# Performance work log

Measured on AMD Instinct MI355X. Metric: run time of the kernel, lower is better.

## Reference

```python
import jax, jax.numpy as jnp
import numpy as np

NUM_USERS = 50000
NUM_ITEMS = 100000
N_NODES = NUM_USERS + NUM_ITEMS
NNZ = 2400000
EMBED = 64
N_LAYERS = 3
BATCH = 4096
NEG_SLOPE = 0.2
EPS = 1e-12


def setup_inputs() -> dict:
    key = jax.random.key(0)
    ks = jax.random.split(key, 12)
    return {
        "edge_val": jax.random.uniform(ks[0], (NNZ,), jnp.float32) * 0.01,
        "embed_user": jax.random.normal(ks[1], (NUM_USERS, EMBED), jnp.float32) * 0.1,
        "embed_item": jax.random.normal(ks[2], (NUM_ITEMS, EMBED), jnp.float32) * 0.1,
        "W1_w": jax.random.normal(ks[3], (N_LAYERS, EMBED, EMBED), jnp.float32) * 0.2,
        "W1_b": jnp.zeros((N_LAYERS, EMBED), jnp.float32),
        "W2_w": jax.random.normal(ks[4], (N_LAYERS, EMBED, EMBED), jnp.float32) * 0.2,
        "W2_b": jnp.zeros((N_LAYERS, EMBED), jnp.float32),
        "edge_row": jax.random.randint(ks[5], (NNZ,), 0, N_NODES, jnp.int32),
        "edge_col": jax.random.randint(ks[6], (NNZ,), 0, N_NODES, jnp.int32),
        "batch_user": jax.random.randint(ks[7], (BATCH,), 0, NUM_USERS, jnp.int32),
        "batch_pos_item": jax.random.randint(ks[8], (BATCH,), 0, NUM_ITEMS, jnp.int32),
        "batch_neg_item": jax.random.randint(ks[9], (BATCH,), 0, NUM_ITEMS, jnp.int32),
    }


def _ngcf_embeddings(edge_val, embed_user, embed_item, W1_w, W1_b, W2_w, W2_b,
                     edge_row, edge_col):
    E = jnp.concatenate([embed_user, embed_item], axis=0)  # [N, d]
    embs = [E]
    for i in range(N_LAYERS):
        # SpMM: (L @ E)[r] = sum over edges e with row r of val[e] * E[col[e]]
        msgs = edge_val[:, None] * E[edge_col]  # [nnz, d]
        LE = jax.ops.segment_sum(msgs, edge_row, num_segments=N_NODES)
        # I is identity -> (L + I) @ E = LE + E
        ego = (LE + E) @ W1_w[i].T + W1_b[i]
        side = LE @ W2_w[i].T + W2_b[i]
        E = jax.nn.leaky_relu(ego + side, negative_slope=NEG_SLOPE)
        # message dropout p=0 is identity; L2-normalize per node (F.normalize)
        norm = jnp.linalg.norm(E, axis=1, keepdims=True)
        E = E / jnp.maximum(norm, EPS)
        embs.append(E)
    return jnp.concatenate(embs, axis=1)  # [N, (1+L)*d]


def reference(edge_val, embed_user, embed_item, W1_w, W1_b, W2_w, W2_b,
              edge_row, edge_col, batch_user, batch_pos_item, batch_neg_item):
    G = _ngcf_embeddings(edge_val, embed_user, embed_item, W1_w, W1_b, W2_w,
                         W2_b, edge_row, edge_col)
    user_g = G[:NUM_USERS]
    item_g = G[NUM_USERS:]
    return (user_g[batch_user], item_g[batch_pos_item], item_g[batch_neg_item])
```

## Files before the change

kernel.cpp:

```cpp
#include <hip/hip_runtime.h>
#include <hip/hip_fp16.h>

#define NUM_USERS 50000
#define NUM_ITEMS 100000
#define N_NODES   150000
#define EMBED     64
#define BATCH     4096
#define NNZ       2400000
#define NB        586
#define CBITS     10
#define NCOARSE   147
#define CAP       20480
#define TILE      4096
#define NTILES    9375

typedef _Float16 half8 __attribute__((ext_vector_type(8)));
typedef float    f32x4 __attribute__((ext_vector_type(4)));

__device__ __forceinline__ float bf2f(unsigned short u) {
    union { unsigned int u32; float f; } v; v.u32 = ((unsigned int)u) << 16; return v.f;
}
__device__ __forceinline__ float getf(const void* p, int i, int fbf) {
    if (fbf) return bf2f(((const unsigned short*)p)[i]);
    return ((const float*)p)[i];
}
__device__ __forceinline__ int geti(const void* p, int i, int i64) {
    if (i64) return (int)(((const long long*)p)[i]);
    return ((const int*)p)[i];
}
__device__ __forceinline__ int clampi(int v, int lo, int hi) {
    return v < lo ? lo : (v > hi ? hi : v);
}
__device__ __forceinline__ float h2f(unsigned short u) {
    return __half2float(__ushort_as_half(u));
}
__device__ __forceinline__ unsigned short f2h(float f) {
    return __half_as_ushort(__float2half(f));
}

__global__ void k_flags_r22(const unsigned short* __restrict__ ev,
                            const void* __restrict__ er, int* __restrict__ fl) {
    if (threadIdx.x == 0 && blockIdx.x == 0) {
        int good = 0;
        for (int i = 0; i < 64; ++i) {
            float f = bf2f(ev[i]);
            if (f >= 0.0f && f <= 0.011f) good++;
        }
        fl[0] = (good >= 60) ? 1 : 0;
        int ok = 0;
        for (int i = 0; i < 64; ++i) {
            long long v = ((const long long*)er)[i];
            if (v >= 0 && v < (long long)N_NODES) ok++;
        }
        fl[1] = (ok >= 60) ? 1 : 0;
    }
}

__global__ void k_probe_r22(int* __restrict__ fl) {
    __shared__ unsigned short A[16 * 32];
    __shared__ unsigned short B[32 * 16];
    const int lane = threadIdx.x;
    for (int i = lane; i < 512; i += 64) {
        int r = i >> 5, k = i & 31;
        A[i] = f2h(((r * 7 + k * 3) % 23) * 0.04f - 0.4f);
    }
    for (int i = lane; i < 512; i += 64) {
        int k = i >> 4, n = i & 15;
        B[i] = f2h(((k * 11 + n * 5) % 19) * 0.05f - 0.45f);
    }
    __syncthreads();
    union { unsigned short u[8]; half8 h; } ua, ub;
    const int rA = lane & 15;
    const int g  = lane >> 4;
    #pragma unroll
    for (int e = 0; e < 8; ++e) {
        ua.u[e] = A[rA * 32 + g * 8 + e];
        ub.u[e] = B[(g * 8 + e) * 16 + rA];
    }
    f32x4 acc = {0.f, 0.f, 0.f, 0.f};
    acc = __builtin_amdgcn_mfma_f32_16x16x32_f16(ua.h, ub.h, acc, 0, 0, 0);
    bool ok = true;
    #pragma unroll
    for (int reg = 0; reg < 4; ++reg) {
        int row = g * 4 + reg;
        int col = lane & 15;
        float ref = 0.0f;
        for (int k = 0; k < 32; ++k)
            ref += h2f(A[row * 32 + k]) * h2f(B[k * 16 + col]);
        if (fabsf(acc[reg] - ref) > 0.02f * fmaxf(1.0f, fabsf(ref))) ok = false;
    }
    unsigned long long m = __ballot(ok);
    if (lane == 0) fl[2] = (m == ~0ull) ? 1 : 0;
}

__global__ void k_init_r22(const void* __restrict__ eu, const void* __restrict__ ei,
                           const int* __restrict__ fl, unsigned short* __restrict__ Eh) {
    int fbf = fl[0];
    int i = blockIdx.x * 256 + threadIdx.x;
    if (i < N_NODES * EMBED) {
        int r = i >> 6;
        float v;
        if (r < NUM_USERS) v = getf(eu, i, fbf);
        else               v = getf(ei, i - NUM_USERS * EMBED, fbf);
        Eh[i] = f2h(v);
    }
}

__global__ __launch_bounds__(256) void k_partA_r22(const void* __restrict__ ev,
                                                   const void* __restrict__ er,
                                                   const void* __restrict__ ec,
                                                   const int* __restrict__ fl,
                                                   int* __restrict__ ccur,
                                                   int2* __restrict__ tmp) {
    __shared__ int2 stage[TILE];
    __shared__ int  hist[NCOARSE];
    __shared__ int  base[NCOARSE];
    const int t   = threadIdx.x;
    const int i64 = fl[1], fbf = fl[0];
    for (int i = t; i < NCOARSE; i += 256) hist[i] = 0;
    __syncthreads();

    int  bx[16], ps[16];
    int2 pk[16];
    const int t0 = blockIdx.x * TILE;
    #pragma unroll
    for (int k = 0; k < 16; ++k) {
        int e = t0 + k * 256 + t;
        bx[k] = -1;
        if (e < NNZ) {
            int r = clampi(geti(er, e, i64), 0, N_NODES - 1);
            int c = clampi(geti(ec, e, i64), 0, N_NODES - 1);
            float v = getf(ev, e, fbf);
            int b = r >> CBITS;
            bx[k] = b;
            pk[k] = make_int2(((r & 1023) << 18) | c, __float_as_int(v));
            ps[k] = atomicAdd(&hist[b], 1);
        }
    }
    __syncthreads();
    if (t == 0) {
        int run = 0;
        for (int i = 0; i < NCOARSE; ++i) { base[i] = run; run += hist[i]; }
    }
    __syncthreads();
    #pragma unroll
    for (int k = 0; k < 16; ++k)
        if (bx[k] >= 0) stage[base[bx[k]] + ps[k]] = pk[k];
    __syncthreads();

    for (int b = t; b < NCOARSE; b += 256) {
        int n = hist[b];
        if (n == 0) continue;
        int g = atomicAdd(&ccur[b], n);
        int2* dst = tmp + (size_t)b * CAP;
        int s0 = base[b];
        for (int i = 0; i < n && (g + i) < CAP; ++i) dst[g + i] = stage[s0 + i];
    }
}

__global__ __launch_bounds__(256) void k_histB1_r22(const int* __restrict__ ccur,
                                                    const int2* __restrict__ tmp,
                                                    int* __restrict__ cnt) {
    __shared__ int h[1024];
    const int b = blockIdx.x;
    const int t = threadIdx.x;
    const int base_row = b << CBITS;
    int nrow = N_NODES - base_row; if (nrow > 1024) nrow = 1024;
    for (int i = t; i < 1024; i += 256) h[i] = 0;
    __syncthreads();
    int n = ccur[b]; if (n > CAP) n = CAP;
    const int2* src = tmp + (size_t)b * CAP;
    for (int p = t; p < n; p += 256) {
        int rl = src[p].x >> 18;
        atomicAdd(&h[rl], 1);
    }
    __syncthreads();
    for (int i = t; i < nrow; i += 256) cnt[base_row + i] = h[i];
}

__global__ __launch_bounds__(256) void k_scanA_r22(const int* __restrict__ cnt,
                                                   int* __restrict__ bsum) {
    int i = blockIdx.x * 256 + threadIdx.x;
    int v = (i < N_NODES) ? cnt[i] : 0;
    #pragma unroll
    for (int d = 1; d < 64; d <<= 1) v += __shfl_xor(v, d, 64);
    __shared__ int sh[4];
    if ((threadIdx.x & 63) == 0) sh[threadIdx.x >> 6] = v;
    __syncthreads();
    if (threadIdx.x == 0) bsum[blockIdx.x] = sh[0] + sh[1] + sh[2] + sh[3];
}

__global__ __launch_bounds__(1024) void k_scanB_r22(int* __restrict__ bsum) {
    __shared__ int sh[1024];
    int t = threadIdx.x;
    if (t < NB) sh[t] = bsum[t];
    __syncthreads();
    if (t == 0) {
        int run = 0;
        for (int i = 0; i < NB; ++i) { int x = sh[i]; sh[i] = run; run += x; }
    }
    __syncthreads();
    if (t < NB) bsum[t] = sh[t];
}

__global__ __launch_bounds__(256) void k_scanC_r22(const int* __restrict__ cnt,
                                                   const int* __restrict__ bsum,
                                                   int* __restrict__ rowptr) {
    __shared__ int sh[256];
    int i = blockIdx.x * 256 + threadIdx.x;
    int t = threadIdx.x;
    sh[t] = (i < N_NODES) ? cnt[i] : 0;
    __syncthreads();
    if (t == 0) {
        int run = bsum[blockIdx.x];
        for (int k = 0; k < 256; ++k) { int x = sh[k]; sh[k] = run; run += x; }
    }
    __syncthreads();
    if (i < N_NODES) rowptr[i] = sh[t];
    if (i == 0) rowptr[N_NODES] = NNZ;
}

__global__ __launch_bounds__(256) void k_place_r22(const int* __restrict__ ccur,
                                                   const int2* __restrict__ tmp,
                                                   const int* __restrict__ rowptr,
                                                   int2* __restrict__ colcv) {
    __shared__ int rp[1025];
    __shared__ int cur[1024];
    const int b = blockIdx.x;
    const int t = threadIdx.x;
    const int base_row = b << CBITS;
    int nrow = N_NODES - base_row; if (nrow > 1024) nrow = 1024;
    for (int i = t; i <= nrow; i += 256) rp[i] = rowptr[base_row + i];
    for (int i = t; i < 1024; i += 256) cur[i] = 0;
    __syncthreads();
    int n = ccur[b]; if (n > CAP) n = CAP;
    const int2* src = tmp + (size_t)b * CAP;
    for (int p = t; p < n; p += 256) {
        int2 cv = src[p];
        int rl = cv.x >> 18;
        int c  = cv.x & 0x3FFFF;
        int dst = rp[rl] + atomicAdd(&cur[rl], 1);
        colcv[dst] = make_int2(c, cv.y);
    }
}

__global__ __launch_bounds__(256) void k_gath_r22(const int* __restrict__ rowptr,
                                                  const int2* __restrict__ colcv,
                                                  const unsigned short* __restrict__ Eh,
                                                  unsigned short* __restrict__ LEh) {
    int r = blockIdx.x * 4 + (threadIdx.x >> 6);
    if (r >= N_NODES) return;
    const int lane = threadIdx.x & 63;
    const int g = lane >> 4;
    const int q = lane & 15;
    const int s = rowptr[r];
    const int e = rowptr[r + 1];

    float a0 = 0.f, a1 = 0.f, a2 = 0.f, a3 = 0.f;

    for (int base = s; base < e; base += 64) {
        int idx = base + lane;
        int2 cv = make_int2(0, 0);
        if (idx < e) cv = colcv[idx];
        int m = e - base; if (m > 64) m = 64;

        for (int j = 0; j < m; j += 8) {
            int i0 = j + g;
            int i1 = j + 4 + g;
            bool v0 = i0 < m;
            bool v1 = i1 < m;
            int   c0 = __shfl(cv.x, i0, 64);
            float f0 = __int_as_float(__shfl(cv.y, i0, 64));
            int   c1 = __shfl(cv.x, i1, 64);
            float f1 = __int_as_float(__shfl(cv.y, i1, 64));
            c0 = v0 ? c0 : 0;  f0 = v0 ? f0 : 0.0f;
            c1 = v1 ? c1 : 0;  f1 = v1 ? f1 : 0.0f;
            ushort4 p0 = *reinterpret_cast<const ushort4*>(&Eh[c0 * EMBED + 4 * q]);
            ushort4 p1 = *reinterpret_cast<const ushort4*>(&Eh[c1 * EMBED + 4 * q]);
            a0 = fmaf(f0, h2f(p0.x), a0);
            a1 = fmaf(f0, h2f(p0.y), a1);
            a2 = fmaf(f0, h2f(p0.z), a2);
            a3 = fmaf(f0, h2f(p0.w), a3);
            a0 = fmaf(f1, h2f(p1.x), a0);
            a1 = fmaf(f1, h2f(p1.y), a1);
            a2 = fmaf(f1, h2f(p1.z), a2);
            a3 = fmaf(f1, h2f(p1.w), a3);
        }
    }

    #pragma unroll
    for (int d = 16; d < 64; d <<= 1) {
        a0 += __shfl_xor(a0, d, 64);
        a1 += __shfl_xor(a1, d, 64);
        a2 += __shfl_xor(a2, d, 64);
        a3 += __shfl_xor(a3, d, 64);
    }
    if (g == 0) {
        ushort4 o;
        o.x = f2h(a0); o.y = f2h(a1); o.z = f2h(a2); o.w = f2h(a3);
        *reinterpret_cast<ushort4*>(&LEh[r * EMBED + 4 * q]) = o;
    }
}

__global__ __launch_bounds__(256) void k_mlp_r22(unsigned short* __restrict__ Eh,
                                                 const unsigned short* __restrict__ LEh,
                                                 const void* __restrict__ W1,
                                                 const void* __restrict__ B1,
                                                 const void* __restrict__ W2,
                                                 const void* __restrict__ B2,
                                                 const int* __restrict__ fl, int layer) {
    __shared__ unsigned short W12s[64 * 72];
    __shared__ unsigned short W1s [64 * 72];
    __shared__ float4 XA[4][16];
    __shared__ float4 XB[4][16];
    const int fbf  = fl[0];
    const int mfok = fl[2];
    const int wofs = layer * EMBED * EMBED;
    const int bofs = layer * EMBED;
    const int t    = threadIdx.x;
    const int lane = t & 63;
    const int w    = t >> 6;

    if (mfok) {
        for (int i = t; i < 4096; i += 256) {
            int n = i >> 6, k = i & 63;
            float w1 = getf(W1, wofs + i, fbf);
            float w2 = getf(W2, wofs + i, fbf);
            W1s [n * 72 + k] = f2h(w1);
            W12s[n * 72 + k] = f2h(w1 + w2);
        }
        __syncthreads();

        const int cl = lane & 15;
        const int g  = lane >> 4;

        float bias[4];
        #pragma unroll
        for (int nt = 0; nt < 4; ++nt)
            bias[nt] = getf(B1, bofs + nt * 16 + cl, fbf) + getf(B2, bofs + nt * 16 + cl, fbf);

        half8 bw12_0[4], bw12_1[4], bw1_0[4], bw1_1[4];
        #pragma unroll
        for (int nt = 0; nt < 4; ++nt) {
            const int nrow = (nt * 16 + cl) * 72;
            bw12_0[nt] = *reinterpret_cast<const half8*>(&W12s[nrow + 0  + g * 8]);
            bw12_1[nt] = *reinterpret_cast<const half8*>(&W12s[nrow + 32 + g * 8]);
            bw1_0 [nt] = *reinterpret_cast<const half8*>(&W1s [nrow + 0  + g * 8]);
            bw1_1 [nt] = *reinterpret_cast<const half8*>(&W1s [nrow + 32 + g * 8]);
        }

        const int gw = blockIdx.x * 4 + w;
        const int nw = gridDim.x * 4;

        for (int tile = gw; tile < NTILES; tile += nw) {
            const int r0 = tile * 16;
            const unsigned short* lerow = &LEh[(r0 + cl) * EMBED];
            const unsigned short* erow  = &Eh [(r0 + cl) * EMBED];
            half8 aLE0 = *reinterpret_cast<const half8*>(&lerow[0  + g * 8]);
            half8 aLE1 = *reinterpret_cast<const half8*>(&lerow[32 + g * 8]);
            half8 aE0  = *reinterpret_cast<const half8*>(&erow [0  + g * 8]);
            half8 aE1  = *reinterpret_cast<const half8*>(&erow [32 + g * 8]);

            f32x4 acc0 = {bias[0], bias[0], bias[0], bias[0]};
            f32x4 acc1 = {bias[1], bias[1], bias[1], bias[1]};
            f32x4 acc2 = {bias[2], bias[2], bias[2], bias[2]};
            f32x4 acc3 = {bias[3], bias[3], bias[3], bias[3]};

            acc0 = __builtin_amdgcn_mfma_f32_16x16x32_f16(aLE0, bw12_0[0], acc0, 0, 0, 0);
            acc1 = __builtin_amdgcn_mfma_f32_16x16x32_f16(aLE0, bw12_0[1], acc1, 0, 0, 0);
            acc2 = __builtin_amdgcn_mfma_f32_16x16x32_f16(aLE0, bw12_0[2], acc2, 0, 0, 0);
            acc3 = __builtin_amdgcn_mfma_f32_16x16x32_f16(aLE0, bw12_0[3], acc3, 0, 0, 0);
            acc0 = __builtin_amdgcn_mfma_f32_16x16x32_f16(aLE1, bw12_1[0], acc0, 0, 0, 0);
            acc1 = __builtin_amdgcn_mfma_f32_16x16x32_f16(aLE1, bw12_1[1], acc1, 0, 0, 0);
            acc2 = __builtin_amdgcn_mfma_f32_16x16x32_f16(aLE1, bw12_1[2], acc2, 0, 0, 0);
            acc3 = __builtin_amdgcn_mfma_f32_16x16x32_f16(aLE1, bw12_1[3], acc3, 0, 0, 0);
            acc0 = __builtin_amdgcn_mfma_f32_16x16x32_f16(aE0,  bw1_0 [0], acc0, 0, 0, 0);
            acc1 = __builtin_amdgcn_mfma_f32_16x16x32_f16(aE0,  bw1_0 [1], acc1, 0, 0, 0);
            acc2 = __builtin_amdgcn_mfma_f32_16x16x32_f16(aE0,  bw1_0 [2], acc2, 0, 0, 0);
            acc3 = __builtin_amdgcn_mfma_f32_16x16x32_f16(aE0,  bw1_0 [3], acc3, 0, 0, 0);
            acc0 = __builtin_amdgcn_mfma_f32_16x16x32_f16(aE1,  bw1_1 [0], acc0, 0, 0, 0);
            acc1 = __builtin_amdgcn_mfma_f32_16x16x32_f16(aE1,  bw1_1 [1], acc1, 0, 0, 0);
            acc2 = __builtin_amdgcn_mfma_f32_16x16x32_f16(aE1,  bw1_1 [2], acc2, 0, 0, 0);
            acc3 = __builtin_amdgcn_mfma_f32_16x16x32_f16(aE1,  bw1_1 [3], acc3, 0, 0, 0);

            f32x4 h0, h1, h2, h3;
            float p0 = 0.f, p1 = 0.f, p2 = 0.f, p3 = 0.f;
            #pragma unroll
            for (int rg = 0; rg < 4; ++rg) {
                float a = acc0[rg]; float hh = (a > 0.f) ? a : 0.2f * a; h0[rg] = hh;
                float s = hh * hh;
                a = acc1[rg]; hh = (a > 0.f) ? a : 0.2f * a; h1[rg] = hh; s += hh * hh;
                a = acc2[rg]; hh = (a > 0.f) ? a : 0.2f * a; h2[rg] = hh; s += hh * hh;
                a = acc3[rg]; hh = (a > 0.f) ? a : 0.2f * a; h3[rg] = hh; s += hh * hh;
                if (rg == 0) p0 = s; else if (rg == 1) p1 = s; else if (rg == 2) p2 = s; else p3 = s;
            }
            #pragma unroll
            for (int d = 1; d < 16; d <<= 1) {
                p0 += __shfl_xor(p0, d, 64);
                p1 += __shfl_xor(p1, d, 64);
                p2 += __shfl_xor(p2, d, 64);
                p3 += __shfl_xor(p3, d, 64);
            }
            float inv0 = 1.0f / fmaxf(sqrtf(p0), 1e-12f);
            float inv1 = 1.0f / fmaxf(sqrtf(p1), 1e-12f);
            float inv2 = 1.0f / fmaxf(sqrtf(p2), 1e-12f);
            float inv3 = 1.0f / fmaxf(sqrtf(p3), 1e-12f);

            #pragma unroll
            for (int rg = 0; rg < 4; ++rg) {
                float inv = (rg == 0) ? inv0 : (rg == 1) ? inv1 : (rg == 2) ? inv2 : inv3;
                unsigned short* orow = &Eh[(r0 + g * 4 + rg) * EMBED + cl];
                orow[0]  = f2h(h0[rg] * inv);
                orow[16] = f2h(h1[rg] * inv);
                orow[32] = f2h(h2[rg] * inv);
                orow[48] = f2h(h3[rg] * inv);
            }
        }
        return;
    }

    float w1r[64], w12r[64];
    if (fbf) {
        const unsigned short* p1 = (const unsigned short*)W1 + wofs + lane * 64;
        const unsigned short* p2 = (const unsigned short*)W2 + wofs + lane * 64;
        #pragma unroll
        for (int q = 0; q < 16; ++q) {
            ushort4 a = reinterpret_cast<const ushort4*>(p1)[q];
            ushort4 b = reinterpret_cast<const ushort4*>(p2)[q];
            float f0 = bf2f(a.x), f1 = bf2f(a.y), f2 = bf2f(a.z), f3 = bf2f(a.w);
            w1r[4*q+0] = f0; w1r[4*q+1] = f1; w1r[4*q+2] = f2; w1r[4*q+3] = f3;
            w12r[4*q+0] = f0 + bf2f(b.x); w12r[4*q+1] = f1 + bf2f(b.y);
            w12r[4*q+2] = f2 + bf2f(b.z); w12r[4*q+3] = f3 + bf2f(b.w);
        }
    } else {
        const float* p1 = (const float*)W1 + wofs + lane * 64;
        const float* p2 = (const float*)W2 + wofs + lane * 64;
        #pragma unroll
        for (int q = 0; q < 16; ++q) {
            float4 a = reinterpret_cast<const float4*>(p1)[q];
            float4 b = reinterpret_cast<const float4*>(p2)[q];
            w1r[4*q+0] = a.x; w1r[4*q+1] = a.y; w1r[4*q+2] = a.z; w1r[4*q+3] = a.w;
            w12r[4*q+0] = a.x + b.x; w12r[4*q+1] = a.y + b.y;
            w12r[4*q+2] = a.z + b.z; w12r[4*q+3] = a.w + b.w;
        }
    }
    const float bias = getf(B1, bofs + lane, fbf) + getf(B2, bofs + lane, fbf);

    const int gw = blockIdx.x * 4 + w;
    const int nw = gridDim.x * 4;

    int row = gw;
    float le = 0.0f, ee = 0.0f;
    if (row < N_NODES) {
        le = h2f(LEh[row * EMBED + lane]);
        ee = h2f(Eh[row * EMBED + lane]);
    }
    while (row < N_NODES) {
        const int nrow = row + nw;
        float nle = 0.0f, nee = 0.0f;
        if (nrow < N_NODES) {
            nle = h2f(LEh[nrow * EMBED + lane]);
            nee = h2f(Eh[nrow * EMBED + lane]);
        }

        ((float*)&XA[w][0])[lane] = le;
        ((float*)&XB[w][0])[lane] = ee;
        float acc0 = bias, acc1 = 0.0f;
        #pragma unroll
        for (int q = 0; q < 16; ++q) {
            float4 a = XA[w][q];
            float4 b = XB[w][q];
            acc0 = fmaf(a.x, w12r[4*q+0], acc0);
            acc1 = fmaf(b.x, w1r [4*q+0], acc1);
            acc0 = fmaf(a.y, w12r[4*q+1], acc0);
            acc1 = fmaf(b.y, w1r [4*q+1], acc1);
            acc0 = fmaf(a.z, w12r[4*q+2], acc0);
            acc1 = fmaf(b.z, w1r [4*q+2], acc1);
            acc0 = fmaf(a.w, w12r[4*q+3], acc0);
            acc1 = fmaf(b.w, w1r [4*q+3], acc1);
        }
        float acc = acc0 + acc1;
        float h = (acc > 0.0f) ? acc : 0.2f * acc;

        float s = h * h;
        #pragma unroll
        for (int d = 1; d < 64; d <<= 1) s += __shfl_xor(s, d, 64);
        const float inv = 1.0f / fmaxf(sqrtf(s), 1e-12f);

        Eh[row * EMBED + lane] = f2h(h * inv);

        row = nrow; le = nle; ee = nee;
    }
}

__global__ void k_pick_r22(const unsigned short* __restrict__ Eh, const void* __restrict__ bu,
                           const void* __restrict__ bp, const void* __restrict__ bn,
                           const int* __restrict__ fl,
                           float* __restrict__ out, int stage) {
    int i64 = fl[1];
    int i = blockIdx.x * 256 + threadIdx.x;
    if (i >= 3 * BATCH * EMBED) return;
    int c = i & 63;
    int row = i >> 6;
    int o = row >> 12;
    int b = row & 4095;
    int idx;
    if (o == 0)      idx = geti(bu, b, i64);
    else if (o == 1) idx = geti(bp, b, i64);
    else             idx = geti(bn, b, i64);
    int src;
    if (o == 0) src = clampi(idx, 0, NUM_USERS - 1);
    else        src = NUM_USERS + clampi(idx, 0, NUM_ITEMS - 1);
    int pos = o * (BATCH * 256) + b * 256 + stage * 64 + c;
    out[pos] = h2f(Eh[src * EMBED + c]);
}

extern "C" void kernel_launch(void* const* d_in, const int* in_sizes, int n_in,
                              void* d_out, int out_size, void* d_ws, size_t ws_size,
                              hipStream_t stream) {
    const void* edge_val = d_in[0];
    const void* emb_u    = d_in[1];
    const void* emb_i    = d_in[2];
    const void* W1w      = d_in[3];
    const void* W1b      = d_in[4];
    const void* W2w      = d_in[5];
    const void* W2b      = d_in[6];
    const void* erow     = d_in[7];
    const void* ecol     = d_in[8];
    const void* bu       = d_in[9];
    const void* bp       = d_in[10];
    const void* bn       = d_in[11];

    const size_t EHB  = (size_t)N_NODES * EMBED * 2;
    const size_t RPB  = 600064;
    const size_t CNB  = 600064;
    const size_t BSB  = 4096;
    const size_t CCB  = 4096;
    const size_t CVB2 = (size_t)NNZ * sizeof(int2);
    const size_t TMPB = (size_t)NCOARSE * CAP * sizeof(int2);

    const size_t need = 256 + 2 * EHB + RPB + CNB + BSB + CCB + CVB2 + TMPB;
    if (ws_size < need) return;

    char* ws = (char*)d_ws;
    int*            fl     = (int*)ws;
    unsigned short* Eh     = (unsigned short*)(ws + 256);
    unsigned short* LEh    = (unsigned short*)(ws + 256 + EHB);
    int*            rowptr = (int*)(ws + 256 + 2 * EHB);
    int*            cnt    = (int*)(ws + 256 + 2 * EHB + RPB);
    int*            bsum   = (int*)(ws + 256 + 2 * EHB + RPB + CNB);
    int*            ccur   = (int*)(ws + 256 + 2 * EHB + RPB + CNB + BSB);
    int2*           colcv  = (int2*)(ws + 256 + 2 * EHB + RPB + CNB + BSB + CCB);
    int2*           tmpcv  = (int2*)(ws + 256 + 2 * EHB + RPB + CNB + BSB + CCB + CVB2);
    float*          out    = (float*)d_out;

    k_flags_r22<<<1, 64, 0, stream>>>((const unsigned short*)edge_val, erow, fl);
    k_probe_r22<<<1, 64, 0, stream>>>(fl);

    k_init_r22<<<(N_NODES * EMBED + 255) / 256, 256, 0, stream>>>(emb_u, emb_i, fl, Eh);

    hipMemsetAsync(ccur, 0, CCB, stream);
    k_partA_r22<<<(NNZ + TILE - 1) / TILE, 256, 0, stream>>>(edge_val, erow, ecol, fl,
                                                             ccur, tmpcv);
    k_histB1_r22<<<NCOARSE, 256, 0, stream>>>(ccur, tmpcv, cnt);
    k_scanA_r22<<<NB, 256, 0, stream>>>(cnt, bsum);
    k_scanB_r22<<<1, 1024, 0, stream>>>(bsum);
    k_scanC_r22<<<NB, 256, 0, stream>>>(cnt, bsum, rowptr);
    k_place_r22<<<NCOARSE, 256, 0, stream>>>(ccur, tmpcv, rowptr, colcv);

    k_pick_r22<<<(3 * BATCH * EMBED + 255) / 256, 256, 0, stream>>>(Eh, bu, bp, bn, fl, out, 0);

    for (int l = 0; l < 3; ++l) {
        k_gath_r22<<<(N_NODES + 3) / 4, 256, 0, stream>>>(rowptr, colcv, Eh, LEh);
        k_mlp_r22<<<2048, 256, 0, stream>>>(Eh, LEh, W1w, W1b, W2w, W2b, fl, l);
        k_pick_r22<<<(3 * BATCH * EMBED + 255) / 256, 256, 0, stream>>>(Eh, bu, bp, bn, fl, out, l + 1);
    }
}
```

Before: 518.4 us.

## Fuse CSR build kernels: merge setup probes, per-bucket scan, histogram and placement

Merges the flag and MFMA-probe kernels and the ccur memset into one setup kernel. The separate histogram, three-stage global scan and placement kernels become a tiny per-bucket prefix kernel plus one fused kernel per coarse bucket. That fused kernel builds the row histogram, scans it locally with the bucket base offset, writes rowptr and scatters the edges. It also cuts the MLP grid from 2048 to 768 blocks. This removes several launches and a pass over the edge buckets, at the cost of a serial 256-step scan inside each placement block.

Measured after the change: 477.8 us. 7.8% less time.

```diff
diff --git a/kernel.cpp b/kernel.cpp
--- a/kernel.cpp
+++ b/kernel.cpp
@@ -7,7 +7,6 @@
 #define EMBED     64
 #define BATCH     4096
 #define NNZ       2400000
-#define NB        586
 #define CBITS     10
 #define NCOARSE   147
 #define CAP       20480
@@ -38,9 +37,16 @@
     return __half_as_ushort(__float2half(f));
 }
 
-__global__ void k_flags_r22(const unsigned short* __restrict__ ev,
-                            const void* __restrict__ er, int* __restrict__ fl) {
-    if (threadIdx.x == 0 && blockIdx.x == 0) {
+__global__ void k_setup_r24(const unsigned short* __restrict__ ev,
+                            const void* __restrict__ er,
+                            int* __restrict__ fl, int* __restrict__ ccur) {
+    __shared__ unsigned short A[16 * 32];
+    __shared__ unsigned short B[32 * 16];
+    const int lane = threadIdx.x;
+
+    for (int i = lane; i < NCOARSE; i += 64) ccur[i] = 0;
+
+    if (lane == 0) {
         int good = 0;
         for (int i = 0; i < 64; ++i) {
             float f = bf2f(ev[i]);
@@ -54,12 +60,7 @@
         }
         fl[1] = (ok >= 60) ? 1 : 0;
     }
-}
-
-__global__ void k_probe_r22(int* __restrict__ fl) {
-    __shared__ unsigned short A[16 * 32];
-    __shared__ unsigned short B[32 * 16];
-    const int lane = threadIdx.x;
+
     for (int i = lane; i < 512; i += 64) {
         int r = i >> 5, k = i & 31;
         A[i] = f2h(((r * 7 + k * 3) % 23) * 0.04f - 0.4f);
@@ -79,7 +80,7 @@
     }
     f32x4 acc = {0.f, 0.f, 0.f, 0.f};
     acc = __builtin_amdgcn_mfma_f32_16x16x32_f16(ua.h, ub.h, acc, 0, 0, 0);
-    bool ok = true;
+    bool ok2 = true;
     #pragma unroll
     for (int reg = 0; reg < 4; ++reg) {
         int row = g * 4 + reg;
@@ -87,13 +88,13 @@
         float ref = 0.0f;
         for (int k = 0; k < 32; ++k)
             ref += h2f(A[row * 32 + k]) * h2f(B[k * 16 + col]);
-        if (fabsf(acc[reg] - ref) > 0.02f * fmaxf(1.0f, fabsf(ref))) ok = false;
-    }
-    unsigned long long m = __ballot(ok);
+        if (fabsf(acc[reg] - ref) > 0.02f * fmaxf(1.0f, fabsf(ref))) ok2 = false;
+    }
+    unsigned long long m = __ballot(ok2);
     if (lane == 0) fl[2] = (m == ~0ull) ? 1 : 0;
 }
 
-__global__ void k_init_r22(const void* __restrict__ eu, const void* __restrict__ ei,
+__global__ void k_init_r24(const void* __restrict__ eu, const void* __restrict__ ei,
                            const int* __restrict__ fl, unsigned short* __restrict__ Eh) {
     int fbf = fl[0];
     int i = blockIdx.x * 256 + threadIdx.x;
@@ -106,7 +107,7 @@
     }
 }
 
-__global__ __launch_bounds__(256) void k_partA_r22(const void* __restrict__ ev,
+__global__ __launch_bounds__(256) void k_partA_r24(const void* __restrict__ ev,
                                                    const void* __restrict__ er,
                                                    const void* __restrict__ ec,
                                                    const int* __restrict__ fl,
@@ -158,93 +159,72 @@
     }
 }
 
-__global__ __launch_bounds__(256) void k_histB1_r22(const int* __restrict__ ccur,
+__global__ void k_bscan_r24(const int* __restrict__ ccur, int* __restrict__ bbase,
+                            int* __restrict__ rowptr) {
+    if (threadIdx.x == 0) {
+        int run = 0;
+        for (int b = 0; b < NCOARSE; ++b) {
+            bbase[b] = run;
+            int n = ccur[b]; if (n > CAP) n = CAP;
+            run += n;
+        }
+        bbase[NCOARSE] = run;
+        rowptr[N_NODES] = run;
+    }
+}
+
+__global__ __launch_bounds__(256) void k_place2_r24(const int* __restrict__ ccur,
+                                                    const int* __restrict__ bbase,
                                                     const int2* __restrict__ tmp,
-                                                    int* __restrict__ cnt) {
+                                                    int2* __restrict__ colcv,
+                                                    int* __restrict__ rowptr) {
     __shared__ int h[1024];
+    __shared__ int rp[1025];
+    __shared__ int part[256];
     const int b = blockIdx.x;
     const int t = threadIdx.x;
     const int base_row = b << CBITS;
     int nrow = N_NODES - base_row; if (nrow > 1024) nrow = 1024;
-    for (int i = t; i < 1024; i += 256) h[i] = 0;
-    __syncthreads();
     int n = ccur[b]; if (n > CAP) n = CAP;
     const int2* src = tmp + (size_t)b * CAP;
-    for (int p = t; p < n; p += 256) {
-        int rl = src[p].x >> 18;
-        atomicAdd(&h[rl], 1);
-    }
-    __syncthreads();
-    for (int i = t; i < nrow; i += 256) cnt[base_row + i] = h[i];
-}
-
-__global__ __launch_bounds__(256) void k_scanA_r22(const int* __restrict__ cnt,
-                                                   int* __restrict__ bsum) {
-    int i = blockIdx.x * 256 + threadIdx.x;
-    int v = (i < N_NODES) ? cnt[i] : 0;
-    #pragma unroll
-    for (int d = 1; d < 64; d <<= 1) v += __shfl_xor(v, d, 64);
-    __shared__ int sh[4];
-    if ((threadIdx.x & 63) == 0) sh[threadIdx.x >> 6] = v;
-    __syncthreads();
-    if (threadIdx.x == 0) bsum[blockIdx.x] = sh[0] + sh[1] + sh[2] + sh[3];
-}
-
-__global__ __launch_bounds__(1024) void k_scanB_r22(int* __restrict__ bsum) {
-    __shared__ int sh[1024];
-    int t = threadIdx.x;
-    if (t < NB) sh[t] = bsum[t];
+    const int bb = bbase[b];
+
+    for (int i = t; i < 1024; i += 256) h[i] = 0;
+    __syncthreads();
+    for (int p = t; p < n; p += 256) atomicAdd(&h[src[p].x >> 18], 1);
+    __syncthreads();
+
+    part[t] = h[4 * t] + h[4 * t + 1] + h[4 * t + 2] + h[4 * t + 3];
     __syncthreads();
     if (t == 0) {
-        int run = 0;
-        for (int i = 0; i < NB; ++i) { int x = sh[i]; sh[i] = run; run += x; }
-    }
-    __syncthreads();
-    if (t < NB) bsum[t] = sh[t];
-}
-
-__global__ __launch_bounds__(256) void k_scanC_r22(const int* __restrict__ cnt,
-                                                   const int* __restrict__ bsum,
-                                                   int* __restrict__ rowptr) {
-    __shared__ int sh[256];
-    int i = blockIdx.x * 256 + threadIdx.x;
-    int t = threadIdx.x;
-    sh[t] = (i < N_NODES) ? cnt[i] : 0;
-    __syncthreads();
-    if (t == 0) {
-        int run = bsum[blockIdx.x];
-        for (int k = 0; k < 256; ++k) { int x = sh[k]; sh[k] = run; run += x; }
-    }
-    __syncthreads();
-    if (i < N_NODES) rowptr[i] = sh[t];
-    if (i == 0) rowptr[N_NODES] = NNZ;
-}
-
-__global__ __launch_bounds__(256) void k_place_r22(const int* __restrict__ ccur,
-                                                   const int2* __restrict__ tmp,
-                                                   const int* __restrict__ rowptr,
-                                                   int2* __restrict__ colcv) {
-    __shared__ int rp[1025];
-    __shared__ int cur[1024];
-    const int b = blockIdx.x;
-    const int t = threadIdx.x;
-    const int base_row = b << CBITS;
-    int nrow = N_NODES - base_row; if (nrow > 1024) nrow = 1024;
-    for (int i = t; i <= nrow; i += 256) rp[i] = rowptr[base_row + i];
-    for (int i = t; i < 1024; i += 256) cur[i] = 0;
-    __syncthreads();
-    int n = ccur[b]; if (n > CAP) n = CAP;
-    const int2* src = tmp + (size_t)b * CAP;
+        int run = bb;
+        for (int i = 0; i < 256; ++i) { int x = part[i]; part[i] = run; run += x; }
+    }
+    __syncthreads();
+    {
+        int run = part[t];
+        rp[4 * t] = run;               run += h[4 * t];
+        rp[4 * t + 1] = run;           run += h[4 * t + 1];
+        rp[4 * t + 2] = run;           run += h[4 * t + 2];
+        rp[4 * t + 3] = run;
+        if (t == 255) rp[1024] = run + h[1023];
+    }
+    __syncthreads();
+
+    for (int i = t; i <= nrow; i += 256) rowptr[base_row + i] = rp[i];
+
+    for (int i = t; i < 1024; i += 256) h[i] = 0;
+    __syncthreads();
     for (int p = t; p < n; p += 256) {
         int2 cv = src[p];
         int rl = cv.x >> 18;
         int c  = cv.x & 0x3FFFF;
-        int dst = rp[rl] + atomicAdd(&cur[rl], 1);
+        int dst = rp[rl] + atomicAdd(&h[rl], 1);
         colcv[dst] = make_int2(c, cv.y);
     }
 }
 
-__global__ __launch_bounds__(256) void k_gath_r22(const int* __restrict__ rowptr,
+__global__ __launch_bounds__(256) void k_gath_r24(const int* __restrict__ rowptr,
                                                   const int2* __restrict__ colcv,
                                                   const unsigned short* __restrict__ Eh,
                                                   unsigned short* __restrict__ LEh) {
@@ -302,7 +282,7 @@
     }
 }
 
-__global__ __launch_bounds__(256) void k_mlp_r22(unsigned short* __restrict__ Eh,
+__global__ __launch_bounds__(256) void k_mlp_r24(unsigned short* __restrict__ Eh,
                                                  const unsigned short* __restrict__ LEh,
                                                  const void* __restrict__ W1,
                                                  const void* __restrict__ B1,
@@ -493,7 +473,7 @@
     }
 }
 
-__global__ void k_pick_r22(const unsigned short* __restrict__ Eh, const void* __restrict__ bu,
+__global__ void k_pick_r24(const unsigned short* __restrict__ Eh, const void* __restrict__ bu,
                            const void* __restrict__ bp, const void* __restrict__ bn,
                            const int* __restrict__ fl,
                            float* __restrict__ out, int stage) {
@@ -533,13 +513,12 @@
 
     const size_t EHB  = (size_t)N_NODES * EMBED * 2;
     const size_t RPB  = 600064;
-    const size_t CNB  = 600064;
-    const size_t BSB  = 4096;
     const size_t CCB  = 4096;
+    const size_t BBB  = 4096;
     const size_t CVB2 = (size_t)NNZ * sizeof(int2);
     const size_t TMPB = (size_t)NCOARSE * CAP * sizeof(int2);
 
-    const size_t need = 256 + 2 * EHB + RPB + CNB + BSB + CCB + CVB2 + TMPB;
+    const size_t need = 256 + 2 * EHB + RPB + CCB + BBB + CVB2 + TMPB;
     if (ws_size < need) return;
 
     char* ws = (char*)d_ws;
@@ -547,32 +526,26 @@
     unsigned short* Eh     = (unsigned short*)(ws + 256);
     unsigned short* LEh    = (unsigned short*)(ws + 256 + EHB);
     int*            rowptr = (int*)(ws + 256 + 2 * EHB);
-    int*            cnt    = (int*)(ws + 256 + 2 * EHB + RPB);
-    int*            bsum   = (int*)(ws + 256 + 2 * EHB + RPB + CNB);
-    int*            ccur   = (int*)(ws + 256 + 2 * EHB + RPB + CNB + BSB);
-    int2*           colcv  = (int2*)(ws + 256 + 2 * EHB + RPB + CNB + BSB + CCB);
-    int2*           tmpcv  = (int2*)(ws + 256 + 2 * EHB + RPB + CNB + BSB + CCB + CVB2);
+    int*            ccur   = (int*)(ws + 256 + 2 * EHB + RPB);
+    int*            bbase  = (int*)(ws + 256 + 2 * EHB + RPB + CCB);
+    int2*           colcv  = (int2*)(ws + 256 + 2 * EHB + RPB + CCB + BBB);
+    int2*           tmpcv  = (int2*)(ws + 256 + 2 * EHB + RPB + CCB + BBB + CVB2);
     float*          out    = (float*)d_out;
 
-    k_flags_r22<<<1, 64, 0, stream>>>((const unsigned short*)edge_val, erow, fl);
-    k_probe_r22<<<1, 64, 0, stream>>>(fl);
-
-    k_init_r22<<<(N_NODES * EMBED + 255) / 256, 256, 0, stream>>>(emb_u, emb_i, fl, Eh);
-
-    hipMemsetAsync(ccur, 0, CCB, stream);
-    k_partA_r22<<<(NNZ + TILE - 1) / TILE, 256, 0, stream>>>(edge_val, erow, ecol, fl,
+    k_setup_r24<<<1, 64, 0, stream>>>((const unsigned short*)edge_val, erow, fl, ccur);
+
+    k_init_r24<<<(N_NODES * EMBED + 255) / 256, 256, 0, stream>>>(emb_u, emb_i, fl, Eh);
+
+    k_partA_r24<<<(NNZ + TILE - 1) / TILE, 256, 0, stream>>>(edge_val, erow, ecol, fl,
                                                              ccur, tmpcv);
-    k_histB1_r22<<<NCOARSE, 256, 0, stream>>>(ccur, tmpcv, cnt);
-    k_scanA_r22<<<NB, 256, 0, stream>>>(cnt, bsum);
-    k_scanB_r22<<<1, 1024, 0, stream>>>(bsum);
-    k_scanC_r22<<<NB, 256, 0, stream>>>(cnt, bsum, rowptr);
-    k_place_r22<<<NCOARSE, 256, 0, stream>>>(ccur, tmpcv, rowptr, colcv);
-
-    k_pick_r22<<<(3 * BATCH * EMBED + 255) / 256, 256, 0, stream>>>(Eh, bu, bp, bn, fl, out, 0);
+    k_bscan_r24<<<1, 64, 0, stream>>>(ccur, bbase, rowptr);
+    k_place2_r24<<<NCOARSE, 256, 0, stream>>>(ccur, bbase, tmpcv, colcv, rowptr);
+
+    k_pick_r24<<<(3 * BATCH * EMBED + 255) / 256, 256, 0, stream>>>(Eh, bu, bp, bn, fl, out, 0);
 
     for (int l = 0; l < 3; ++l) {
-        k_gath_r22<<<(N_NODES + 3) / 4, 256, 0, stream>>>(rowptr, colcv, Eh, LEh);
-        k_mlp_r22<<<2048, 256, 0, stream>>>(Eh, LEh, W1w, W1b, W2w, W2b, fl, l);
-        k_pick_r22<<<(3 * BATCH * EMBED + 255) / 256, 256, 0, stream>>>(Eh, bu, bp, bn, fl, out, l + 1);
-    }
-}
+        k_gath_r24<<<(N_NODES + 3) / 4, 256, 0, stream>>>(rowptr, colcv, Eh, LEh);
+        k_mlp_r24<<<768, 256, 0, stream>>>(Eh, LEh, W1w, W1b, W2w, W2b, fl, l);
+        k_pick_r24<<<(3 * BATCH * EMBED + 255) / 256, 256, 0, stream>>>(Eh, bu, bp, bn, fl, out, l + 1);
+    }
+}
```
